# Optimization experiments

Hardware: AMD Instinct MI355X
Metric: run time of the kernel (lower is better)

The kernel has to match this reference:

```python
import jax, jax.numpy as jnp
import numpy as np

EPS = 1e-5
SLOPE = 0.01  # torch LeakyReLU default

def _conv(x, w, b, stride):
    # x: [B,C,L], w: [O,I,3]
    y = jax.lax.conv_general_dilated(x, w, (stride,), [(1, 1)],
                                     dimension_numbers=("NCH", "OIH", "NCH"))
    return y + b[None, :, None]

def _bn(x, g, b, m, v):
    # eval-mode BatchNorm1d with running stats
    inv = jax.lax.rsqrt(v + EPS)
    return (x - m[None, :, None]) * (g * inv)[None, :, None] + b[None, :, None]

def _lrelu(x):
    return jnp.where(x >= 0, x, SLOPE * x)

def setup_inputs() -> dict:
    key = jax.random.key(0)
    ks = jax.random.split(key, 32)
    B, C, L = 32, 256, 2048
    K, D = 4096, 128
    d = {}
    d["x"] = jax.random.normal(ks[0], (B, C, L), dtype=jnp.float32)
    # conv weights [O,I,3]
    d["w1"] = jax.random.normal(ks[1], (256, 256, 3), jnp.float32) * 0.03
    d["b1"] = jax.random.normal(ks[2], (256,), jnp.float32) * 0.01
    d["w2"] = jax.random.normal(ks[3], (512, 256, 3), jnp.float32) * 0.03
    d["b2"] = jax.random.normal(ks[4], (512,), jnp.float32) * 0.01
    d["w3"] = jax.random.normal(ks[5], (512, 512, 3), jnp.float32) * 0.02
    d["b3"] = jax.random.normal(ks[6], (512,), jnp.float32) * 0.01
    d["w4"] = jax.random.normal(ks[7], (D, 512, 3), jnp.float32) * 0.02
    d["b4"] = jax.random.normal(ks[8], (D,), jnp.float32) * 0.01
    for i, ch in enumerate([256, 512, 512, D]):
        d[f"g{i+1}"] = 1.0 + 0.1 * jax.random.normal(ks[9 + 4 * i], (ch,), jnp.float32)
        d[f"be{i+1}"] = 0.1 * jax.random.normal(ks[10 + 4 * i], (ch,), jnp.float32)
        d[f"m{i+1}"] = 0.1 * jax.random.normal(ks[11 + 4 * i], (ch,), jnp.float32)
        d[f"v{i+1}"] = 0.5 + jax.random.uniform(ks[12 + 4 * i], (ch,), jnp.float32)
    d["emb"] = jax.random.uniform(ks[30], (K, D), jnp.float32,
                                  minval=-1.0 / K, maxval=1.0 / K)
    return d

def reference(x, w1, b1, w2, b2, w3, b3, w4, b4,
              g1, be1, m1, v1, g2, be2, m2, v2,
              g3, be3, m3, v3, g4, be4, m4, v4, emb):
    h = _lrelu(_bn(_conv(x, w1, b1, 2), g1, be1, m1, v1))   # [B,256,L/2]
    h = _lrelu(_bn(_conv(h, w2, b2, 2), g2, be2, m2, v2))   # [B,512,L/4]
    h = _lrelu(_bn(_conv(h, w3, b3, 2), g3, be3, m3, v3))   # [B,512,L/8]
    h = _lrelu(_bn(_conv(h, w4, b4, 1), g4, be4, m4, v4))   # [B,D,L/8]
    flat = jnp.transpose(h, (0, 2, 1)).reshape(-1, h.shape[1])  # [N,D]
    # squared-distance expansion: ||f||^2 + ||e||^2 - 2 f.e
    dist = (jnp.sum(flat * flat, axis=1, keepdims=True)
            + jnp.sum(emb * emb, axis=1)
            - 2.0 * flat @ emb.T)                            # [N,K]
    codes = jnp.argmin(dist, axis=1)
    return codes, dist
```

## Files before the change

### kernel.cpp

```cpp
#include <hip/hip_runtime.h>
#include <cstdint>
#include <math.h>

#define EPS_BN 1e-5f
#define SLOPE 0.01f
#define C14 6.103515625e-5f
#define SC14 16384.0f
#define HMIN 6.103515625e-5f

typedef __attribute__((ext_vector_type(8))) _Float16 half8;
typedef __attribute__((ext_vector_type(8))) short short8;
typedef __attribute__((ext_vector_type(16))) float f32x16;
typedef __attribute__((ext_vector_type(4))) float f32x4;

__device__ __forceinline__ void split16(float v, unsigned short& uh,
                                        unsigned short& ul) {
    _Float16 h = (_Float16)v;
    if (fabsf(v) < HMIN) h = (_Float16)0.0f;
    float rem = v - (float)h;
    _Float16 l = (_Float16)(rem * SC14);
    uh = __builtin_bit_cast(unsigned short, h);
    ul = __builtin_bit_cast(unsigned short, l);
}

__global__ __launch_bounds__(256)
void wprep_all(const float* __restrict__ w1, short* __restrict__ o1,
               const float* __restrict__ w2, short* __restrict__ o2,
               const float* __restrict__ w3, short* __restrict__ o3,
               const float* __restrict__ w4, short* __restrict__ o4)
{
    const float* w; short* wbuf; int CIN, COUT;
    switch (blockIdx.y) {
        case 0: w = w1; wbuf = o1; CIN = 256; COUT = 256; break;
        case 1: w = w2; wbuf = o2; CIN = 256; COUT = 512; break;
        case 2: w = w3; wbuf = o3; CIN = 512; COUT = 512; break;
        default: w = w4; wbuf = o4; CIN = 512; COUT = 128; break;
    }
    int KST = CIN / 16, OB = COUT / 128;
    int total = KST * OB * 1536;
    for (int sid = blockIdx.x * 256 + threadIdx.x; sid < total;
         sid += gridDim.x * 256) {
        int slot = sid % 1536;
        int kb = sid / 1536;
        int ob = kb % OB, ks = kb / OB;
        int m = slot & 31, hi = (slot >> 5) & 1, mf = (slot >> 6) & 3;
        int ts = slot >> 8;
        int t = ts >> 1, s = ts & 1;
        int oc = ob * 128 + mf * 32 + m;
        int ib = ks * 16 + hi * 8;
        short8 r;
        #pragma unroll
        for (int j = 0; j < 8; ++j) {
            float v = w[((size_t)oc * CIN + ib + j) * 3 + t];
            unsigned short uh, ul;
            split16(v, uh, ul);
            r[j] = (short)(s == 0 ? uh : ul);
        }
        *(short8*)(wbuf + (size_t)sid * 8) = r;
    }
}

__global__ __launch_bounds__(256)
void bnprep_init(
    const float* __restrict__ g1, const float* __restrict__ be1,
    const float* __restrict__ m1, const float* __restrict__ v1,
    const float* __restrict__ b1, float* __restrict__ sc1, float* __restrict__ off1,
    const float* __restrict__ g2, const float* __restrict__ be2,
    const float* __restrict__ m2, const float* __restrict__ v2,
    const float* __restrict__ b2, float* __restrict__ sc2, float* __restrict__ off2,
    const float* __restrict__ g3, const float* __restrict__ be3,
    const float* __restrict__ m3, const float* __restrict__ v3,
    const float* __restrict__ b3, float* __restrict__ sc3, float* __restrict__ off3,
    const float* __restrict__ g4, const float* __restrict__ be4,
    const float* __restrict__ m4, const float* __restrict__ v4,
    const float* __restrict__ b4, float* __restrict__ sc4, float* __restrict__ off4,
    unsigned long long* __restrict__ mp, float* __restrict__ sf)
{
    int bid = blockIdx.x;
    if (bid >= 38) { sf[(bid - 38) * 256 + threadIdx.x] = 0.0f; return; }
    if (bid >= 6) { mp[(bid - 6) * 256 + threadIdx.x] = ~0ULL; return; }
    const float *g, *be, *m, *v, *bias;
    float *sc, *off;
    int c;
    if (bid == 0) {
        g = g1; be = be1; m = m1; v = v1; bias = b1; sc = sc1; off = off1;
        c = threadIdx.x;
    } else if (bid <= 2) {
        g = g2; be = be2; m = m2; v = v2; bias = b2; sc = sc2; off = off2;
        c = (bid - 1) * 256 + threadIdx.x;
    } else if (bid <= 4) {
        g = g3; be = be3; m = m3; v = v3; bias = b3; sc = sc3; off = off3;
        c = (bid - 3) * 256 + threadIdx.x;
    } else {
        g = g4; be = be4; m = m4; v = v4; bias = b4; sc = sc4; off = off4;
        c = threadIdx.x;
        if (c >= 128) return;
    }
    float s = g[c] / sqrtf(v[c] + EPS_BN);
    sc[c] = s;
    off[c] = (bias[c] - m[c]) * s + be[c];
}

template<int CIN, int COUT, int LIN, int TILE, int EPI, int SRC>
__global__ __launch_bounds__(512, 1)
void conv_pair(const short* __restrict__ wbuf, const short* __restrict__ xpl,
               const float* __restrict__ xraw,
               const float* __restrict__ scv, const float* __restrict__ offv,
               short* __restrict__ opl)
{
    constexpr int LOUT = LIN / 2;
    constexpr int KST = CIN / 16;
    constexpr int OBS = COUT / 128;
    constexpr int NG = CIN / 8;
    constexpr int SLOTS = LIN / 2 + 1;
    constexpr size_t PLIN = (size_t)32 * NG * 2 * SLOTS * 8;
    constexpr int NF = TILE / 64;
    constexpr int NGo = COUT / 8;
    constexpr int OSLOTS = (EPI == 0) ? (LOUT / 2 + 1) : (LOUT + 2);
    constexpr size_t PLOUT = (size_t)32 * NGo * ((EPI == 0) ? 2 : 1) * OSLOTS * 8;

    constexpr int XOFF = 49152;
    constexpr int BUF  = XOFF + 8 * 2112;
    constexpr int SCOFF = 2 * BUF;
    __shared__ __align__(16) char lds[2 * BUF + 2048];

    const int tid = threadIdx.x;
    const int lane = tid & 63;
    const int wv = tid >> 6;
    const int wo = wv >> 2;
    const int wm = (wv >> 1) & 1, wn = wv & 1;
    const int hi = lane >> 5, n32 = lane & 31;
    const int n0 = blockIdx.x * TILE;
    const int oby = blockIdx.y;
    const int o0 = oby * 256;
    const int b = blockIdx.z;

    if (tid < 256) ((float*)(lds + SCOFF))[tid] = scv[o0 + tid];
    else ((float*)(lds + SCOFF + 1024))[tid - 256] = offv[o0 + tid - 256];

    f32x16 acc0[2][2], acc1[2][2];
    #pragma unroll
    for (int i = 0; i < 2; ++i)
        #pragma unroll
        for (int j = 0; j < 2; ++j)
            #pragma unroll
            for (int e = 0; e < 16; ++e) { acc0[i][j][e] = 0.0f; acc1[i][j][e] = 0.0f; }

    short8 rw[6];
    short8 rxa, rxb, rxc;
    float rf[8], rf2[8];

    auto stage_load = [&](int ks) {
        const short* wsrc = wbuf + ((size_t)ks * OBS + (oby * 2 + wo)) * 1536 * 8;
        #pragma unroll
        for (int it = 0; it < 6; ++it)
            rw[it] = *(const short8*)(wsrc +
                      (size_t)(it * 256 + (wv & 3) * 64 + lane) * 8);
        if constexpr (SRC == 0) {
            int sg = wv >> 2, rhi = (wv >> 1) & 1, arr = wv & 1;
            int start = arr ? n0 : (n0 + 1);
            const short* src = xpl + (size_t)sg * PLIN
                + ((((size_t)b * NG + (ks * 2 + rhi)) * 2 + arr) * SLOTS + start) * 8;
            rxa = *(const short8*)(src + (size_t)lane * 8);
            if constexpr (TILE == 128) {
                rxb = *(const short8*)(src + (size_t)(64 + lane) * 8);
                if (arr && lane == 0)
                    rxc = *(const short8*)(src + (size_t)128 * 8);
            } else {
                if (arr && lane == 0)
                    rxb = *(const short8*)(src + (size_t)64 * 8);
            }
        } else {
            int run = wv & 3, rhi = run >> 1, arr = run & 1, hs = wv >> 2;
            int c = hs * 64 + lane;
            int l = arr ? (2 * (n0 + c) - 1) : (2 * (n0 + c));
            const float* xr = xraw + ((size_t)(b * 256 + ks * 16 + rhi * 8)) * 2048;
            #pragma unroll
            for (int j = 0; j < 8; ++j)
                rf[j] = (l >= 0) ? xr[(size_t)j * 2048 + l] : 0.0f;
            if (arr && hs == 1 && lane == 0) {
                int l2 = 2 * (n0 + 128) - 1;
                #pragma unroll
                for (int j = 0; j < 8; ++j)
                    rf2[j] = xr[(size_t)j * 2048 + l2];
            }
        }
    };

    auto stage_write = [&](char* base) {
        #pragma unroll
        for (int it = 0; it < 6; ++it)
            *(short8*)(base + wo * 24576 +
                       (it * 256 + (wv & 3) * 64 + lane) * 16) = rw[it];
        if constexpr (SRC == 0) {
            int sg = wv >> 2, rhi = (wv >> 1) & 1, arr = wv & 1;
            char* dst = base + XOFF + ((sg * 2 + rhi) * 2 + arr) * 2112;
            *(short8*)(dst + lane * 16) = rxa;
            if constexpr (TILE == 128) {
                *(short8*)(dst + (64 + lane) * 16) = rxb;
                if (arr && lane == 0) *(short8*)(dst + 128 * 16) = rxc;
            } else {
                if (arr && lane == 0) *(short8*)(dst + 64 * 16) = rxb;
            }
        } else {
            int run = wv & 3, rhi = run >> 1, arr = run & 1, hs = wv >> 2;
            int c = hs * 64 + lane;
            short8 rh, rl;
            #pragma unroll
            for (int j = 0; j < 8; ++j) {
                unsigned short uh, ul;
                split16(rf[j], uh, ul);
                rh[j] = (short)uh; rl[j] = (short)ul;
            }
            char* dst = base + XOFF + (rhi * 2 + arr) * 2112;
            *(short8*)(dst + c * 16) = rh;
            *(short8*)(dst + 8448 + c * 16) = rl;
            if (arr && hs == 1 && lane == 0) {
                short8 rh2, rl2;
                #pragma unroll
                for (int j = 0; j < 8; ++j) {
                    unsigned short uh, ul;
                    split16(rf2[j], uh, ul);
                    rh2[j] = (short)uh; rl2[j] = (short)ul;
                }
                *(short8*)(dst + 128 * 16) = rh2;
                *(short8*)(dst + 8448 + 128 * 16) = rl2;
            }
        }
    };

    stage_load(0);
    stage_write(lds);
    __syncthreads();

    #pragma unroll 1
    for (int ks = 0; ks < KST; ++ks) {
        const char* cbase = lds + (ks & 1) * BUF;
        bool more = (ks + 1 < KST);
        if (more) stage_load(ks + 1);
        __builtin_amdgcn_s_setprio(1);
        #pragma unroll
        for (int t = 0; t < 3; ++t) {
            half8 af[2][2], bx[2][2];
            #pragma unroll
            for (int s = 0; s < 2; ++s) {
                #pragma unroll
                for (int mf = 0; mf < 2; ++mf)
                    af[s][mf] = *(const half8*)(cbase + wo * 24576 +
                        (((t * 2 + s) * 4 + (wm * 2 + mf)) * 64 + lane) * 16);
                int arr = (t == 1) ? 0 : 1;
                int tof = (t == 2) ? 1 : 0;
                #pragma unroll
                for (int nf = 0; nf < NF; ++nf) {
                    int qb = wn * (TILE / 2) + nf * 32 + tof;
                    bx[s][nf] = *(const half8*)(cbase + XOFF + s * 8448
                                                + arr * 2112 + qb * 16
                                                + hi * 4224 + n32 * 16);
                }
            }
            #pragma unroll
            for (int mf = 0; mf < 2; ++mf)
                #pragma unroll
                for (int nf = 0; nf < NF; ++nf) {
                    acc0[mf][nf] = __builtin_amdgcn_mfma_f32_32x32x16_f16(
                        af[0][mf], bx[0][nf], acc0[mf][nf], 0, 0, 0);
                    acc1[mf][nf] = __builtin_amdgcn_mfma_f32_32x32x16_f16(
                        af[0][mf], bx[1][nf], acc1[mf][nf], 0, 0, 0);
                    acc1[mf][nf] = __builtin_amdgcn_mfma_f32_32x32x16_f16(
                        af[1][mf], bx[0][nf], acc1[mf][nf], 0, 0, 0);
                }
        }
        __builtin_amdgcn_s_setprio(0);
        if (more) stage_write(lds + ((ks + 1) & 1) * BUF);
        __syncthreads();
    }

    #pragma unroll
    for (int half = 0; half < NF; ++half) {
        __syncthreads();
        #pragma unroll
        for (int mf = 0; mf < 2; ++mf)
            #pragma unroll
            for (int r = 0; r < 16; ++r) {
                int ocl = mf * 32 + (r & 3) + 8 * (r >> 2) + 4 * hi;
                *(float*)(lds + wv * 8704 + n32 * 272 + ocl * 4) =
                    acc0[mf][half][r] + C14 * acc1[mf][half][r];
            }
        __syncthreads();
        #pragma unroll
        for (int it = 0; it < 4; ++it) {
            int sl = tid + it * 512;
            int w = sl >> 8, rem = sl & 255, p = rem >> 3, grp = rem & 7;
            int wo_ = w >> 2, wm_ = (w >> 1) & 1, wn_ = w & 1;
            f32x4 v0 = *(f32x4*)(lds + w * 8704 + p * 272 + grp * 32);
            f32x4 v1 = *(f32x4*)(lds + w * 8704 + p * 272 + grp * 32 + 16);
            int ocb = wo_ * 128 + wm_ * 64 + grp * 8;
            f32x4 s0 = *(f32x4*)(lds + SCOFF + ocb * 4);
            f32x4 s1 = *(f32x4*)(lds + SCOFF + ocb * 4 + 16);
            f32x4 q0 = *(f32x4*)(lds + SCOFF + 1024 + ocb * 4);
            f32x4 q1 = *(f32x4*)(lds + SCOFF + 1024 + ocb * 4 + 16);
            float y[8];
            #pragma unroll
            for (int j = 0; j < 4; ++j) {
                float a = v0[j] * s0[j] + q0[j];
                y[j] = a >= 0.0f ? a : SLOPE * a;
                float c = v1[j] * s1[j] + q1[j];
                y[4 + j] = c >= 0.0f ? c : SLOPE * c;
            }
            int pos_abs = n0 + wn_ * (TILE / 2) + half * 32 + p;
            int oc_abs = o0 + ocb;
            short8 rh, rl;
            #pragma unroll
            for (int j = 0; j < 8; ++j) {
                unsigned short uh, ul;
                split16(y[j], uh, ul);
                rh[j] = (short)uh; rl[j] = (short)ul;
            }
            int gq = oc_abs >> 3;
            size_t base;
            if (EPI == 0) {
                int arr = pos_abs & 1;
                int slot = arr ? (pos_abs + 1) / 2 : pos_abs / 2 + 1;
                base = ((((size_t)b * NGo + gq) * 2 + arr) * OSLOTS + slot) * 8;
            } else {
                base = (((size_t)b * NGo + gq) * OSLOTS + (pos_abs + 1)) * 8;
            }
            *(short8*)(opl + base) = rh;
            *(short8*)(opl + PLOUT + base) = rl;
        }
    }

    if (EPI == 0) {
        if (blockIdx.x == 0 && tid < 128) {
            int sg = tid >> 6, r2 = tid & 63, g16 = r2 >> 1, a2 = r2 & 1;
            int gq = oby * 32 + g16;
            short8 z;
            #pragma unroll
            for (int j = 0; j < 8; ++j) z[j] = 0;
            *(short8*)(opl + (size_t)sg * PLOUT +
                       ((((size_t)b * NGo + gq) * 2 + a2) * OSLOTS) * 8) = z;
        }
    } else {
        if (tid < 64 && (blockIdx.x == 0 || blockIdx.x == gridDim.x - 1)) {
            int sg = tid >> 5, g16 = tid & 31;
            int gq = oby * 32 + g16;
            int slot = (blockIdx.x == 0) ? 0 : (OSLOTS - 1);
            short8 z;
            #pragma unroll
            for (int j = 0; j < 8; ++j) z[j] = 0;
            *(short8*)(opl + (size_t)sg * PLOUT +
                       (((size_t)b * NGo + gq) * OSLOTS + slot) * 8) = z;
        }
    }
}

template<int CIN, int COUT, int LIN>
__global__ __launch_bounds__(256, 2)
void conv_s1(const short* __restrict__ wbuf, const short* __restrict__ xpl,
             const float* __restrict__ scv, const float* __restrict__ offv,
             short* __restrict__ fh, short* __restrict__ fl,
             float* __restrict__ sf)
{
    constexpr int KST = CIN / 16;
    constexpr int NG = CIN / 8;
    constexpr int SLOTS = LIN + 2;
    constexpr size_t PLIN = (size_t)32 * NG * SLOTS * 8;
    constexpr int TILE = 64;

    constexpr int XOFF = 24576;
    constexpr int BUF  = XOFF + 4 * 2112;
    constexpr int SCOFF = 2 * BUF;
    __shared__ __align__(16) char lds[2 * BUF + 1024];

    const int tid = threadIdx.x;
    const int lane = tid & 63;
    const int wv = tid >> 6;
    const int wm = wv >> 1, wn = wv & 1;
    const int hi = lane >> 5, n32 = lane & 31;
    const int n0 = blockIdx.x * TILE;
    const int b = blockIdx.z;

    if (tid < 128) {
        ((float*)(lds + SCOFF))[tid] = scv[tid];
        ((float*)(lds + SCOFF + 512))[tid] = offv[tid];
    }

    f32x16 acc0[2], acc1[2];
    #pragma unroll
    for (int i = 0; i < 2; ++i)
        #pragma unroll
        for (int e = 0; e < 16; ++e) { acc0[i][e] = 0.0f; acc1[i][e] = 0.0f; }

    short8 rw[6], rxa, rxb;

    auto stage_load = [&](int ks) {
        const short* wsrc = wbuf + (size_t)ks * 1536 * 8;
        #pragma unroll
        for (int it = 0; it < 6; ++it)
            rw[it] = *(const short8*)(wsrc +
                      (size_t)(it * 256 + wv * 64 + lane) * 8);
        int sg = wv >> 1, rhi = wv & 1;
        const short* src = xpl + (size_t)sg * PLIN
            + (((size_t)b * NG + (ks * 2 + rhi)) * SLOTS + n0) * 8;
        rxa = *(const short8*)(src + (size_t)lane * 8);
        if (lane < 2) rxb = *(const short8*)(src + (size_t)(64 + lane) * 8);
    };
    auto stage_write = [&](char* base) {
        #pragma unroll
        for (int it = 0; it < 6; ++it)
            *(short8*)(base + (it * 256 + wv * 64 + lane) * 16) = rw[it];
        int sg = wv >> 1, rhi = wv & 1;
        char* dst = base + XOFF + (sg * 2 + rhi) * 2112;
        *(short8*)(dst + lane * 16) = rxa;
        if (lane < 2) *(short8*)(dst + (64 + lane) * 16) = rxb;
    };

    stage_load(0);
    stage_write(lds);
    __syncthreads();

    #pragma unroll 1
    for (int ks = 0; ks < KST; ++ks) {
        const char* cbase = lds + (ks & 1) * BUF;
        bool more = (ks + 1 < KST);
        if (more) stage_load(ks + 1);
        __builtin_amdgcn_s_setprio(1);
        #pragma unroll
        for (int t = 0; t < 3; ++t) {
            half8 af[2][2], bx[2];
            #pragma unroll
            for (int s = 0; s < 2; ++s) {
                #pragma unroll
                for (int mf = 0; mf < 2; ++mf)
                    af[s][mf] = *(const half8*)(cbase +
                        (((t * 2 + s) * 4 + (wm * 2 + mf)) * 64 + lane) * 16);
                int qb = wn * 32 + t;
                bx[s] = *(const half8*)(cbase + XOFF + s * 4224
                                        + qb * 16 + hi * 2112 + n32 * 16);
            }
            #pragma unroll
            for (int mf = 0; mf < 2; ++mf) {
                acc0[mf] = __builtin_amdgcn_mfma_f32_32x32x16_f16(
                    af[0][mf], bx[0], acc0[mf], 0, 0, 0);
                acc1[mf] = __builtin_amdgcn_mfma_f32_32x32x16_f16(
                    af[0][mf], bx[1], acc1[mf], 0, 0, 0);
                acc1[mf] = __builtin_amdgcn_mfma_f32_32x32x16_f16(
                    af[1][mf], bx[0], acc1[mf], 0, 0, 0);
            }
        }
        __builtin_amdgcn_s_setprio(0);
        if (more) stage_write(lds + ((ks + 1) & 1) * BUF);
        __syncthreads();
    }

    __syncthreads();
    #pragma unroll
    for (int mf = 0; mf < 2; ++mf)
        #pragma unroll
        for (int r = 0; r < 16; ++r) {
            int ocl = mf * 32 + (r & 3) + 8 * (r >> 2) + 4 * hi;
            *(float*)(lds + wv * 8704 + n32 * 272 + ocl * 4) =
                acc0[mf][r] + C14 * acc1[mf][r];
        }
    __syncthreads();
    #pragma unroll
    for (int it = 0; it < 4; ++it) {
        int sl = tid + it * 256;
        int w = sl >> 8, rem = sl & 255, p = rem >> 3, grp = rem & 7;
        int wm_ = w >> 1, wn_ = w & 1;
        f32x4 v0 = *(f32x4*)(lds + w * 8704 + p * 272 + grp * 32);
        f32x4 v1 = *(f32x4*)(lds + w * 8704 + p * 272 + grp * 32 + 16);
        int oclb = wm_ * 64 + grp * 8;
        f32x4 s0 = *(f32x4*)(lds + SCOFF + oclb * 4);
        f32x4 s1 = *(f32x4*)(lds + SCOFF + oclb * 4 + 16);
        f32x4 q0 = *(f32x4*)(lds + SCOFF + 512 + oclb * 4);
        f32x4 q1 = *(f32x4*)(lds + SCOFF + 512 + oclb * 4 + 16);
        float y[8];
        #pragma unroll
        for (int j = 0; j < 4; ++j) {
            float a = v0[j] * s0[j] + q0[j];
            y[j] = a >= 0.0f ? a : SLOPE * a;
            float c = v1[j] * s1[j] + q1[j];
            y[4 + j] = c >= 0.0f ? c : SLOPE * c;
        }
        int pos_abs = n0 + wn_ * 32 + p;
        int n = b * 256 + pos_abs;
        short8 rh, rl;
        float partial = 0.0f;
        #pragma unroll
        for (int j = 0; j < 8; ++j) {
            partial = fmaf(y[j], y[j], partial);
            unsigned short uh, ul;
            split16(y[j], uh, ul);
            rh[j] = (short)uh; rl[j] = (short)ul;
        }
        int g = wm_ * 8 + grp;
        size_t slot = ((((size_t)(n >> 5) * 8 + (g >> 1)) * 2 + (g & 1)) * 32
                       + (n & 31)) * 8;
        *(short8*)(fh + slot) = rh;
        *(short8*)(fl + slot) = rl;
        atomicAdd(sf + n, partial);
    }
}

__global__ __launch_bounds__(256)
void split_kernel(const float* __restrict__ src, int nrows,
                  short* __restrict__ ph, short* __restrict__ pl,
                  float* __restrict__ sumv)
{
    int t = blockIdx.x * 256 + threadIdx.x;
    int n = t >> 4, g = t & 15;
    if (n >= nrows) return;
    const float* rowp = src + (size_t)n * 128 + g * 8;
    float4 v0 = *(const float4*)rowp;
    float4 v1 = *(const float4*)(rowp + 4);
    float vv[8] = {v0.x, v0.y, v0.z, v0.w, v1.x, v1.y, v1.z, v1.w};
    short8 rh, rl;
    float ss = 0.0f;
    #pragma unroll
    for (int j = 0; j < 8; ++j) {
        float v = vv[j];
        ss = fmaf(v, v, ss);
        unsigned short uh, ul;
        split16(v, uh, ul);
        rh[j] = (short)uh; rl[j] = (short)ul;
    }
    int nb = n >> 5, m = n & 31, ks = g >> 1, hi = g & 1;
    size_t slot = ((((size_t)nb * 8 + ks) * 2 + hi) * 32 + m) * 8;
    *(short8*)(ph + slot) = rh;
    *(short8*)(pl + slot) = rl;
    #pragma unroll
    for (int mk = 8; mk; mk >>= 1) ss += __shfl_xor(ss, mk);
    if (g == 0) sumv[n] = ss;
}

__global__ __launch_bounds__(256, 2)
void distmin_kernel(const short* __restrict__ fh, const short* __restrict__ fl,
                    const short* __restrict__ eh, const short* __restrict__ el,
                    const float* __restrict__ sf, const float* __restrict__ se,
                    float* __restrict__ dist, unsigned long long* __restrict__ mp)
{
    __shared__ unsigned long long cand[128 * 64];
    const int tid = threadIdx.x;
    const int lane = tid & 63;
    const int wv = tid >> 6;
    const int wm = wv >> 1, wn = wv & 1;
    const int hi = lane >> 5, n32 = lane & 31;
    const int kb = blockIdx.x;
    const int nb = blockIdx.y;

    f32x16 acc0[2][2], acc1[2][2];
    #pragma unroll
    for (int i = 0; i < 2; ++i)
        #pragma unroll
        for (int j = 0; j < 2; ++j)
            #pragma unroll
            for (int e = 0; e < 16; ++e) { acc0[i][j][e] = 0.0f; acc1[i][j][e] = 0.0f; }

    const short* fb[2][2];
    const short* eb[2][2];
    {
        const short* fpl[2] = {fh, fl};
        const short* epl[2] = {eh, el};
        #pragma unroll
        for (int s = 0; s < 2; ++s) {
            #pragma unroll
            for (int mf = 0; mf < 2; ++mf)
                fb[s][mf] = fpl[s] + (size_t)nb * 16384
                            + ((size_t)(wm * 2 + mf) * 8 * 64 + lane) * 8;
            #pragma unroll
            for (int nf = 0; nf < 2; ++nf)
                eb[s][nf] = epl[s]
                            + ((size_t)(kb * 4 + wn * 2 + nf) * 8 * 64 + lane) * 8;
        }
    }

    #pragma unroll
    for (int ks = 0; ks < 8; ++ks) {
        half8 af[2][2], bx[2][2];
        #pragma unroll
        for (int s = 0; s < 2; ++s) {
            #pragma unroll
            for (int mf = 0; mf < 2; ++mf)
                af[s][mf] = *(const half8*)(fb[s][mf] + ks * 512);
            #pragma unroll
            for (int nf = 0; nf < 2; ++nf)
                bx[s][nf] = *(const half8*)(eb[s][nf] + ks * 512);
        }
        #pragma unroll
        for (int mf = 0; mf < 2; ++mf)
            #pragma unroll
            for (int nf = 0; nf < 2; ++nf) {
                acc0[mf][nf] = __builtin_amdgcn_mfma_f32_32x32x16_f16(
                    af[0][mf], bx[0][nf], acc0[mf][nf], 0, 0, 0);
                acc1[mf][nf] = __builtin_amdgcn_mfma_f32_32x32x16_f16(
                    af[0][mf], bx[1][nf], acc1[mf][nf], 0, 0, 0);
                acc1[mf][nf] = __builtin_amdgcn_mfma_f32_32x32x16_f16(
                    af[1][mf], bx[0][nf], acc1[mf][nf], 0, 0, 0);
            }
    }

    const int n_blk = nb * 128;
    const int kc0 = kb * 128 + wn * 64 + n32;
    const float se0 = se[kc0];
    const float se1 = se[kc0 + 32];
    #pragma unroll
    for (int mf = 0; mf < 2; ++mf) {
        #pragma unroll
        for (int r = 0; r < 16; ++r) {
            int nloc = wm * 64 + mf * 32 + (r & 3) + 8 * (r >> 2) + 4 * hi;
            int n = n_blk + nloc;
            float sfn = sf[n];
            float d0 = acc0[mf][0][r] + C14 * acc1[mf][0][r];
            float d1 = acc0[mf][1][r] + C14 * acc1[mf][1][r];
            float v0 = (sfn + se0) - 2.0f * d0;
            float v1 = (sfn + se1) - 2.0f * d1;
            __builtin_nontemporal_store(v0, &dist[(size_t)n * 4096 + kc0]);
            __builtin_nontemporal_store(v1, &dist[(size_t)n * 4096 + kc0 + 32]);
            unsigned long long p0 =
                (((unsigned long long)__float_as_uint(v0)) << 32) | (unsigned)kc0;
            unsigned long long p1 =
                (((unsigned long long)__float_as_uint(v1)) << 32) | (unsigned)(kc0 + 32);
            unsigned long long p = p1 < p0 ? p1 : p0;
            cand[nloc * 64 + wn * 32 + n32] = p;
        }
    }
    __syncthreads();
    {
        int row = tid >> 1, h = tid & 1;
        unsigned long long best = ~0ULL;
        #pragma unroll
        for (int i = 0; i < 32; ++i) {
            int c = h * 32 + ((i + row) & 31);
            unsigned long long cv = cand[row * 64 + c];
            best = cv < best ? cv : best;
        }
        unsigned lo = (unsigned)best, hw = (unsigned)(best >> 32);
        unsigned lo2 = __shfl_xor(lo, 1), hw2 = __shfl_xor(hw, 1);
        unsigned long long ob = (((unsigned long long)hw2) << 32) | lo2;
        if (ob < best) best = ob;
        if (h == 0) atomicMin(mp + n_blk + row, best);
    }
}

__global__ __launch_bounds__(256)
void codes_kernel(const unsigned long long* __restrict__ mp,
                  float* __restrict__ codes)
{
    int n = blockIdx.x * 256 + threadIdx.x;
    if (n < 8192) codes[n] = (float)(unsigned)(mp[n] & 0xffffffffULL);
}

extern "C" void kernel_launch(void* const* d_in, const int* in_sizes, int n_in,
                              void* d_out, int out_size, void* d_ws, size_t ws_size,
                              hipStream_t stream)
{
    const float* x   = (const float*)d_in[0];
    const float* w1  = (const float*)d_in[1];
    const float* b1  = (const float*)d_in[2];
    const float* w2  = (const float*)d_in[3];
    const float* b2  = (const float*)d_in[4];
    const float* w3  = (const float*)d_in[5];
    const float* b3  = (const float*)d_in[6];
    const float* w4  = (const float*)d_in[7];
    const float* b4  = (const float*)d_in[8];
    const float* g1  = (const float*)d_in[9];
    const float* be1 = (const float*)d_in[10];
    const float* m1  = (const float*)d_in[11];
    const float* v1  = (const float*)d_in[12];
    const float* g2  = (const float*)d_in[13];
    const float* be2 = (const float*)d_in[14];
    const float* m2  = (const float*)d_in[15];
    const float* v2  = (const float*)d_in[16];
    const float* g3  = (const float*)d_in[17];
    const float* be3 = (const float*)d_in[18];
    const float* m3  = (const float*)d_in[19];
    const float* v3  = (const float*)d_in[20];
    const float* g4  = (const float*)d_in[21];
    const float* be4 = (const float*)d_in[22];
    const float* m4  = (const float*)d_in[23];
    const float* v4  = (const float*)d_in[24];
    const float* emb = (const float*)d_in[25];

    float* outf  = (float*)d_out;
    float* codes = outf;
    float* distm = outf + 8192;

    char* wsb = (char*)d_ws;
    short* wb1 = (short*)(wsb + 0);
    short* wb2 = (short*)(wsb + 786432);
    short* wb3 = (short*)(wsb + 2359296);
    short* wb4 = (short*)(wsb + 5505024);
    float* sc1 = (float*)(wsb + 6291456); float* off1 = sc1 + 256;
    float* sc2 = (float*)(wsb + 6293504); float* off2 = sc2 + 512;
    float* sc3 = (float*)(wsb + 6297600); float* off3 = sc3 + 512;
    float* sc4 = (float*)(wsb + 6301696); float* off4 = sc4 + 128;
    short* h1p = (short*)(wsb + 6302720);
    short* fh  = (short*)(wsb + 39922688);
    short* fl  = (short*)(wsb + 42019840);
    short* eh  = (short*)(wsb + 44116992);
    short* el  = (short*)(wsb + 45165568);
    float* sf  = (float*)(wsb + 46214144);
    float* se  = (float*)(wsb + 46246912);
    unsigned long long* mp = (unsigned long long*)(wsb + 46263296);

    char* db = (char*)distm;
    short* h2p = (short*)db;
    short* h3p = (short*)(db + 33685504);

    wprep_all<<<dim3(192, 4), 256, 0, stream>>>(w1, wb1, w2, wb2, w3, wb3, w4, wb4);
    bnprep_init<<<70, 256, 0, stream>>>(
        g1, be1, m1, v1, b1, sc1, off1,
        g2, be2, m2, v2, b2, sc2, off2,
        g3, be3, m3, v3, b3, sc3, off3,
        g4, be4, m4, v4, b4, sc4, off4, mp, sf);
    split_kernel<<<256, 256, 0, stream>>>(emb, 4096, eh, el, se);

    conv_pair<256, 256, 2048, 128, 0, 1>
        <<<dim3(8, 1, 32), 512, 0, stream>>>(wb1, nullptr, x, sc1, off1, h1p);
    conv_pair<256, 512, 1024, 128, 0, 0>
        <<<dim3(4, 2, 32), 512, 0, stream>>>(wb2, h1p, nullptr, sc2, off2, h2p);
    conv_pair<512, 512, 512, 64, 1, 0>
        <<<dim3(4, 2, 32), 512, 0, stream>>>(wb3, h2p, nullptr, sc3, off3, h3p);
    conv_s1<512, 128, 256>
        <<<dim3(4, 1, 32), 256, 0, stream>>>(wb4, h3p, sc4, off4, fh, fl, sf);

    distmin_kernel<<<dim3(32, 64), 256, 0, stream>>>(fh, fl, eh, el,
                                                     sf, se, distm, mp);
    codes_kernel<<<32, 256, 0, stream>>>(mp, codes);
}
```

Baseline: 235.1 us.

## Replace LDS-staged conv kernels with a direct-global-load generalized conv kernel

Generalizes the stride-1 conv kernel into conv_ng, which handles stride-2 and stride-1 layers with configurable tile and epilogue, and uses it for conv layers 2-4 in place of conv_pair and conv_s1. The main loop no longer double-buffers weights and activations through shared memory; each wave loads its MFMA fragments straight from global memory, relying on cache, and unrolls by two. Output channels are split across blockIdx.y in 128-wide blocks, with 256-thread blocks instead of 512. This removes LDS staging and barriers from the K loop, at the cost of redundant global or L2 traffic and more exposed load latency.

Result: slower. 306.8 us (+30.5%).

```diff
diff --git a/kernel.cpp b/kernel.cpp
--- a/kernel.cpp
+++ b/kernel.cpp
@@ -354,23 +354,28 @@
     }
 }
 
-template<int CIN, int COUT, int LIN>
-__global__ __launch_bounds__(256, 2)
-void conv_s1(const short* __restrict__ wbuf, const short* __restrict__ xpl,
+template<int CIN, int COUT, int LIN, int STRIDE, int TILE, int EPI>
+__global__ __launch_bounds__(256)
+void conv_ng(const short* __restrict__ wbuf, const short* __restrict__ xpl,
              const float* __restrict__ scv, const float* __restrict__ offv,
-             short* __restrict__ fh, short* __restrict__ fl,
-             float* __restrict__ sf)
+             short* __restrict__ opl, short* __restrict__ fh,
+             short* __restrict__ fl, float* __restrict__ sf)
 {
+    constexpr int LOUT = LIN / STRIDE;
     constexpr int KST = CIN / 16;
+    constexpr int OBS = COUT / 128;
     constexpr int NG = CIN / 8;
-    constexpr int SLOTS = LIN + 2;
-    constexpr size_t PLIN = (size_t)32 * NG * SLOTS * 8;
-    constexpr int TILE = 64;
-
-    constexpr int XOFF = 24576;
-    constexpr int BUF  = XOFF + 4 * 2112;
-    constexpr int SCOFF = 2 * BUF;
-    __shared__ __align__(16) char lds[2 * BUF + 1024];
+    constexpr int NARR = (STRIDE == 2) ? 2 : 1;
+    constexpr int SLOTS = (STRIDE == 2) ? (LIN / 2 + 1) : (LIN + 2);
+    constexpr size_t PLIN = (size_t)32 * NG * NARR * SLOTS * 8;
+    constexpr int PW = TILE / 2;
+    constexpr int NF = PW / 32;
+    constexpr int NGo = COUT / 8;
+    constexpr int OSLOTS = (EPI == 0) ? (LOUT / 2 + 1) : (LOUT + 2);
+    constexpr size_t PLOUT = (size_t)32 * NGo * ((EPI == 0) ? 2 : 1) * OSLOTS * 8;
+
+    constexpr int SCOFF = 4 * 8704;
+    __shared__ __align__(16) char lds[SCOFF + 1024];
 
     const int tid = threadIdx.x;
     const int lane = tid & 63;
@@ -378,128 +383,158 @@
     const int wm = wv >> 1, wn = wv & 1;
     const int hi = lane >> 5, n32 = lane & 31;
     const int n0 = blockIdx.x * TILE;
+    const int ob = blockIdx.y;
+    const int o0 = ob * 128;
     const int b = blockIdx.z;
 
     if (tid < 128) {
-        ((float*)(lds + SCOFF))[tid] = scv[tid];
-        ((float*)(lds + SCOFF + 512))[tid] = offv[tid];
-    }
-
-    f32x16 acc0[2], acc1[2];
+        ((float*)(lds + SCOFF))[tid] = scv[o0 + tid];
+        ((float*)(lds + SCOFF + 512))[tid] = offv[o0 + tid];
+    }
+
+    f32x16 acc0[2][NF], acc1[2][NF];
     #pragma unroll
     for (int i = 0; i < 2; ++i)
         #pragma unroll
-        for (int e = 0; e < 16; ++e) { acc0[i][e] = 0.0f; acc1[i][e] = 0.0f; }
-
-    short8 rw[6], rxa, rxb;
-
-    auto stage_load = [&](int ks) {
-        const short* wsrc = wbuf + (size_t)ks * 1536 * 8;
-        #pragma unroll
-        for (int it = 0; it < 6; ++it)
-            rw[it] = *(const short8*)(wsrc +
-                      (size_t)(it * 256 + wv * 64 + lane) * 8);
-        int sg = wv >> 1, rhi = wv & 1;
-        const short* src = xpl + (size_t)sg * PLIN
-            + (((size_t)b * NG + (ks * 2 + rhi)) * SLOTS + n0) * 8;
-        rxa = *(const short8*)(src + (size_t)lane * 8);
-        if (lane < 2) rxb = *(const short8*)(src + (size_t)(64 + lane) * 8);
-    };
-    auto stage_write = [&](char* base) {
-        #pragma unroll
-        for (int it = 0; it < 6; ++it)
-            *(short8*)(base + (it * 256 + wv * 64 + lane) * 16) = rw[it];
-        int sg = wv >> 1, rhi = wv & 1;
-        char* dst = base + XOFF + (sg * 2 + rhi) * 2112;
-        *(short8*)(dst + lane * 16) = rxa;
-        if (lane < 2) *(short8*)(dst + (64 + lane) * 16) = rxb;
-    };
-
-    stage_load(0);
-    stage_write(lds);
-    __syncthreads();
-
-    #pragma unroll 1
+        for (int j = 0; j < NF; ++j)
+            #pragma unroll
+            for (int e = 0; e < 16; ++e) { acc0[i][j][e] = 0.0f; acc1[i][j][e] = 0.0f; }
+
+    const short* wb = wbuf + ((size_t)ob * 1536 + wm * 128 + lane) * 8;
+    constexpr size_t WKS = (size_t)OBS * 1536 * 8;
+
+    size_t xslot0;
+    if constexpr (STRIDE == 2)
+        xslot0 = ((size_t)(b * NG + hi) * 2) * SLOTS + n0 + wn * PW + n32;
+    else
+        xslot0 = ((size_t)(b * NG + hi)) * SLOTS + n0 + wn * PW + n32;
+    const short* xb = xpl + xslot0 * 8;
+    constexpr size_t XKS = (size_t)((STRIDE == 2) ? 4 : 2) * SLOTS * 8;
+
+    #pragma unroll 2
     for (int ks = 0; ks < KST; ++ks) {
-        const char* cbase = lds + (ks & 1) * BUF;
-        bool more = (ks + 1 < KST);
-        if (more) stage_load(ks + 1);
-        __builtin_amdgcn_s_setprio(1);
+        const short* wk = wb + (size_t)ks * WKS;
+        const short* xk = xb + (size_t)ks * XKS;
+        half8 af[3][2][2], bx[3][2][NF];
         #pragma unroll
         for (int t = 0; t < 3; ++t) {
-            half8 af[2][2], bx[2];
+            constexpr int XT2[3] = {SLOTS, 1, SLOTS + 1};
+            int xt = (STRIDE == 2) ? XT2[t] : t;
             #pragma unroll
             for (int s = 0; s < 2; ++s) {
                 #pragma unroll
                 for (int mf = 0; mf < 2; ++mf)
-                    af[s][mf] = *(const half8*)(cbase +
-                        (((t * 2 + s) * 4 + (wm * 2 + mf)) * 64 + lane) * 16);
-                int qb = wn * 32 + t;
-                bx[s] = *(const half8*)(cbase + XOFF + s * 4224
-                                        + qb * 16 + hi * 2112 + n32 * 16);
-            }
-            #pragma unroll
-            for (int mf = 0; mf < 2; ++mf) {
-                acc0[mf] = __builtin_amdgcn_mfma_f32_32x32x16_f16(
-                    af[0][mf], bx[0], acc0[mf], 0, 0, 0);
-                acc1[mf] = __builtin_amdgcn_mfma_f32_32x32x16_f16(
-                    af[0][mf], bx[1], acc1[mf], 0, 0, 0);
-                acc1[mf] = __builtin_amdgcn_mfma_f32_32x32x16_f16(
-                    af[1][mf], bx[0], acc1[mf], 0, 0, 0);
-            }
-        }
-        __builtin_amdgcn_s_setprio(0);
-        if (more) stage_write(lds + ((ks + 1) & 1) * BUF);
+                    af[t][s][mf] = *(const half8*)(wk +
+                        ((size_t)((t * 2 + s) * 256 + mf * 64)) * 8);
+                #pragma unroll
+                for (int nf = 0; nf < NF; ++nf)
+                    bx[t][s][nf] = *(const half8*)(xk + (size_t)s * PLIN
+                                                   + (size_t)(xt + nf * 32) * 8);
+            }
+        }
+        #pragma unroll
+        for (int t = 0; t < 3; ++t)
+            #pragma unroll
+            for (int mf = 0; mf < 2; ++mf)
+                #pragma unroll
+                for (int nf = 0; nf < NF; ++nf) {
+                    acc0[mf][nf] = __builtin_amdgcn_mfma_f32_32x32x16_f16(
+                        af[t][0][mf], bx[t][0][nf], acc0[mf][nf], 0, 0, 0);
+                    acc1[mf][nf] = __builtin_amdgcn_mfma_f32_32x32x16_f16(
+                        af[t][0][mf], bx[t][1][nf], acc1[mf][nf], 0, 0, 0);
+                    acc1[mf][nf] = __builtin_amdgcn_mfma_f32_32x32x16_f16(
+                        af[t][1][mf], bx[t][0][nf], acc1[mf][nf], 0, 0, 0);
+                }
+    }
+
+    #pragma unroll
+    for (int half = 0; half < NF; ++half) {
         __syncthreads();
-    }
-
-    __syncthreads();
-    #pragma unroll
-    for (int mf = 0; mf < 2; ++mf)
-        #pragma unroll
-        for (int r = 0; r < 16; ++r) {
-            int ocl = mf * 32 + (r & 3) + 8 * (r >> 2) + 4 * hi;
-            *(float*)(lds + wv * 8704 + n32 * 272 + ocl * 4) =
-                acc0[mf][r] + C14 * acc1[mf][r];
-        }
-    __syncthreads();
-    #pragma unroll
-    for (int it = 0; it < 4; ++it) {
-        int sl = tid + it * 256;
-        int w = sl >> 8, rem = sl & 255, p = rem >> 3, grp = rem & 7;
-        int wm_ = w >> 1, wn_ = w & 1;
-        f32x4 v0 = *(f32x4*)(lds + w * 8704 + p * 272 + grp * 32);
-        f32x4 v1 = *(f32x4*)(lds + w * 8704 + p * 272 + grp * 32 + 16);
-        int oclb = wm_ * 64 + grp * 8;
-        f32x4 s0 = *(f32x4*)(lds + SCOFF + oclb * 4);
-        f32x4 s1 = *(f32x4*)(lds + SCOFF + oclb * 4 + 16);
-        f32x4 q0 = *(f32x4*)(lds + SCOFF + 512 + oclb * 4);
-        f32x4 q1 = *(f32x4*)(lds + SCOFF + 512 + oclb * 4 + 16);
-        float y[8];
-        #pragma unroll
-        for (int j = 0; j < 4; ++j) {
-            float a = v0[j] * s0[j] + q0[j];
-            y[j] = a >= 0.0f ? a : SLOPE * a;
-            float c = v1[j] * s1[j] + q1[j];
-            y[4 + j] = c >= 0.0f ? c : SLOPE * c;
-        }
-        int pos_abs = n0 + wn_ * 32 + p;
-        int n = b * 256 + pos_abs;
-        short8 rh, rl;
-        float partial = 0.0f;
-        #pragma unroll
-        for (int j = 0; j < 8; ++j) {
-            partial = fmaf(y[j], y[j], partial);
-            unsigned short uh, ul;
-            split16(y[j], uh, ul);
-            rh[j] = (short)uh; rl[j] = (short)ul;
-        }
-        int g = wm_ * 8 + grp;
-        size_t slot = ((((size_t)(n >> 5) * 8 + (g >> 1)) * 2 + (g & 1)) * 32
-                       + (n & 31)) * 8;
-        *(short8*)(fh + slot) = rh;
-        *(short8*)(fl + slot) = rl;
-        atomicAdd(sf + n, partial);
+        #pragma unroll
+        for (int mf = 0; mf < 2; ++mf)
+            #pragma unroll
+            for (int r = 0; r < 16; ++r) {
+                int ocl = mf * 32 + (r & 3) + 8 * (r >> 2) + 4 * hi;
+                *(float*)(lds + wv * 8704 + n32 * 272 + ocl * 4) =
+                    acc0[mf][half][r] + C14 * acc1[mf][half][r];
+            }
+        __syncthreads();
+        #pragma unroll
+        for (int it = 0; it < 4; ++it) {
+            int sl = tid + it * 256;
+            int w = sl >> 8, rem = sl & 255, p = rem >> 3, grp = rem & 7;
+            int wm_ = w >> 1, wn_ = w & 1;
+            f32x4 v0 = *(f32x4*)(lds + w * 8704 + p * 272 + grp * 32);
+            f32x4 v1 = *(f32x4*)(lds + w * 8704 + p * 272 + grp * 32 + 16);
+            int ocb = wm_ * 64 + grp * 8;
+            f32x4 s0 = *(f32x4*)(lds + SCOFF + ocb * 4);
+            f32x4 s1 = *(f32x4*)(lds + SCOFF + ocb * 4 + 16);
+            f32x4 q0 = *(f32x4*)(lds + SCOFF + 512 + ocb * 4);
+            f32x4 q1 = *(f32x4*)(lds + SCOFF + 512 + ocb * 4 + 16);
+            float y[8];
+            #pragma unroll
+            for (int j = 0; j < 4; ++j) {
+                float a = v0[j] * s0[j] + q0[j];
+                y[j] = a >= 0.0f ? a : SLOPE * a;
+                float c = v1[j] * s1[j] + q1[j];
+                y[4 + j] = c >= 0.0f ? c : SLOPE * c;
+            }
+            int pos_abs = n0 + wn_ * PW + half * 32 + p;
+            int oc_abs = o0 + ocb;
+            short8 rh, rl;
+            float partial = 0.0f;
+            #pragma unroll
+            for (int j = 0; j < 8; ++j) {
+                if (EPI == 2) partial = fmaf(y[j], y[j], partial);
+                unsigned short uh, ul;
+                split16(y[j], uh, ul);
+                rh[j] = (short)uh; rl[j] = (short)ul;
+            }
+            if constexpr (EPI == 2) {
+                int n = b * 256 + pos_abs;
+                int g = oc_abs >> 3;
+                size_t slot = ((((size_t)(n >> 5) * 8 + (g >> 1)) * 2 + (g & 1)) * 32
+                               + (n & 31)) * 8;
+                *(short8*)(fh + slot) = rh;
+                *(short8*)(fl + slot) = rl;
+                atomicAdd(sf + n, partial);
+            } else {
+                int gq = oc_abs >> 3;
+                size_t base;
+                if (EPI == 0) {
+                    int arr = pos_abs & 1;
+                    int slot = arr ? (pos_abs + 1) / 2 : pos_abs / 2 + 1;
+                    base = ((((size_t)b * NGo + gq) * 2 + arr) * OSLOTS + slot) * 8;
+                } else {
+                    base = (((size_t)b * NGo + gq) * OSLOTS + (pos_abs + 1)) * 8;
+                }
+                *(short8*)(opl + base) = rh;
+                *(short8*)(opl + PLOUT + base) = rl;
+            }
+        }
+    }
+
+    if constexpr (EPI == 0) {
+        if (blockIdx.x == 0 && tid < 64) {
+            int sg = tid >> 5, r2 = tid & 31, g16 = r2 >> 1, a2 = r2 & 1;
+            int gq = ob * 16 + g16;
+            short8 z;
+            #pragma unroll
+            for (int j = 0; j < 8; ++j) z[j] = 0;
+            *(short8*)(opl + (size_t)sg * PLOUT +
+                       ((((size_t)b * NGo + gq) * 2 + a2) * OSLOTS) * 8) = z;
+        }
+    } else if constexpr (EPI == 1) {
+        if (tid < 32 && (blockIdx.x == 0 || blockIdx.x == gridDim.x - 1)) {
+            int sg = tid >> 4, g16 = tid & 15;
+            int gq = ob * 16 + g16;
+            int slot = (blockIdx.x == 0) ? 0 : (OSLOTS - 1);
+            short8 z;
+            #pragma unroll
+            for (int j = 0; j < 8; ++j) z[j] = 0;
+            *(short8*)(opl + (size_t)sg * PLOUT +
+                       (((size_t)b * NGo + gq) * OSLOTS + slot) * 8) = z;
+        }
     }
 }
 
@@ -718,12 +753,15 @@
 
     conv_pair<256, 256, 2048, 128, 0, 1>
         <<<dim3(8, 1, 32), 512, 0, stream>>>(wb1, nullptr, x, sc1, off1, h1p);
-    conv_pair<256, 512, 1024, 128, 0, 0>
-        <<<dim3(4, 2, 32), 512, 0, stream>>>(wb2, h1p, nullptr, sc2, off2, h2p);
-    conv_pair<512, 512, 512, 64, 1, 0>
-        <<<dim3(4, 2, 32), 512, 0, stream>>>(wb3, h2p, nullptr, sc3, off3, h3p);
-    conv_s1<512, 128, 256>
-        <<<dim3(4, 1, 32), 256, 0, stream>>>(wb4, h3p, sc4, off4, fh, fl, sf);
+    conv_ng<256, 512, 1024, 2, 128, 0>
+        <<<dim3(4, 4, 32), 256, 0, stream>>>(wb2, h1p, sc2, off2, h2p,
+                                             nullptr, nullptr, nullptr);
+    conv_ng<512, 512, 512, 2, 128, 1>
+        <<<dim3(2, 4, 32), 256, 0, stream>>>(wb3, h2p, sc3, off3, h3p,
+                                             nullptr, nullptr, nullptr);
+    conv_ng<512, 128, 256, 1, 64, 2>
+        <<<dim3(4, 1, 32), 256, 0, stream>>>(wb4, h3p, sc4, off4, nullptr,
+                                             fh, fl, sf);
 
     distmin_kernel<<<dim3(32, 64), 256, 0, stream>>>(fh, fl, eh, el,
                                                      sf, se, distm, mp);
```

## Load conv weight fragments directly from global memory instead of staging through LDS

Applied to the files above, without the earlier changes.

Both conv kernels stop staging the weight tile through registers into double-buffered shared memory. Each wave now reads its MFMA A-fragments straight from global memory inside the inner loop, and only the activation tile stays in LDS. This removes the weight LDS writes and reads and shrinks the shared-memory footprint. In exchange, weight loads are no longer prefetched one stage ahead, so global or L2 latency lands directly in the MFMA loop, and waves sharing weights issue redundant global reads.

Result: slower. 313.1 us (+33.2%).

```diff
diff --git a/kernel.cpp b/kernel.cpp
--- a/kernel.cpp
+++ b/kernel.cpp
@@ -119,10 +119,9 @@
     constexpr int OSLOTS = (EPI == 0) ? (LOUT / 2 + 1) : (LOUT + 2);
     constexpr size_t PLOUT = (size_t)32 * NGo * ((EPI == 0) ? 2 : 1) * OSLOTS * 8;
 
-    constexpr int XOFF = 49152;
-    constexpr int BUF  = XOFF + 8 * 2112;
-    constexpr int SCOFF = 2 * BUF;
-    __shared__ __align__(16) char lds[2 * BUF + 2048];
+    constexpr int BUF  = 8 * 2112;
+    constexpr int SCOFF = 8 * 8704;
+    __shared__ __align__(16) char lds[SCOFF + 2048];
 
     const int tid = threadIdx.x;
     const int lane = tid & 63;
@@ -146,16 +145,13 @@
             #pragma unroll
             for (int e = 0; e < 16; ++e) { acc0[i][j][e] = 0.0f; acc1[i][j][e] = 0.0f; }
 
-    short8 rw[6];
+    const short* wkb = wbuf + ((size_t)(oby * 2 + wo) * 1536 + lane) * 8;
+    constexpr size_t WKS = (size_t)OBS * 1536 * 8;
+
     short8 rxa, rxb, rxc;
     float rf[8], rf2[8];
 
     auto stage_load = [&](int ks) {
-        const short* wsrc = wbuf + ((size_t)ks * OBS + (oby * 2 + wo)) * 1536 * 8;
-        #pragma unroll
-        for (int it = 0; it < 6; ++it)
-            rw[it] = *(const short8*)(wsrc +
-                      (size_t)(it * 256 + (wv & 3) * 64 + lane) * 8);
         if constexpr (SRC == 0) {
             int sg = wv >> 2, rhi = (wv >> 1) & 1, arr = wv & 1;
             int start = arr ? n0 : (n0 + 1);
@@ -188,13 +184,9 @@
     };
 
     auto stage_write = [&](char* base) {
-        #pragma unroll
-        for (int it = 0; it < 6; ++it)
-            *(short8*)(base + wo * 24576 +
-                       (it * 256 + (wv & 3) * 64 + lane) * 16) = rw[it];
         if constexpr (SRC == 0) {
             int sg = wv >> 2, rhi = (wv >> 1) & 1, arr = wv & 1;
-            char* dst = base + XOFF + ((sg * 2 + rhi) * 2 + arr) * 2112;
+            char* dst = base + ((sg * 2 + rhi) * 2 + arr) * 2112;
             *(short8*)(dst + lane * 16) = rxa;
             if constexpr (TILE == 128) {
                 *(short8*)(dst + (64 + lane) * 16) = rxb;
@@ -212,7 +204,7 @@
                 split16(rf[j], uh, ul);
                 rh[j] = (short)uh; rl[j] = (short)ul;
             }
-            char* dst = base + XOFF + (rhi * 2 + arr) * 2112;
+            char* dst = base + (rhi * 2 + arr) * 2112;
             *(short8*)(dst + c * 16) = rh;
             *(short8*)(dst + 8448 + c * 16) = rl;
             if (arr && hs == 1 && lane == 0) {
@@ -236,6 +228,7 @@
     #pragma unroll 1
     for (int ks = 0; ks < KST; ++ks) {
         const char* cbase = lds + (ks & 1) * BUF;
+        const short* wk = wkb + (size_t)ks * WKS;
         bool more = (ks + 1 < KST);
         if (more) stage_load(ks + 1);
         __builtin_amdgcn_s_setprio(1);
@@ -246,14 +239,14 @@
             for (int s = 0; s < 2; ++s) {
                 #pragma unroll
                 for (int mf = 0; mf < 2; ++mf)
-                    af[s][mf] = *(const half8*)(cbase + wo * 24576 +
-                        (((t * 2 + s) * 4 + (wm * 2 + mf)) * 64 + lane) * 16);
+                    af[s][mf] = *(const half8*)(wk +
+                        (size_t)(((t * 2 + s) * 4 + (wm * 2 + mf)) * 64) * 8);
                 int arr = (t == 1) ? 0 : 1;
                 int tof = (t == 2) ? 1 : 0;
                 #pragma unroll
                 for (int nf = 0; nf < NF; ++nf) {
                     int qb = wn * (TILE / 2) + nf * 32 + tof;
-                    bx[s][nf] = *(const half8*)(cbase + XOFF + s * 8448
+                    bx[s][nf] = *(const half8*)(cbase + s * 8448
                                                 + arr * 2112 + qb * 16
                                                 + hi * 4224 + n32 * 16);
                 }
@@ -367,10 +360,9 @@
     constexpr size_t PLIN = (size_t)32 * NG * SLOTS * 8;
     constexpr int TILE = 64;
 
-    constexpr int XOFF = 24576;
-    constexpr int BUF  = XOFF + 4 * 2112;
-    constexpr int SCOFF = 2 * BUF;
-    __shared__ __align__(16) char lds[2 * BUF + 1024];
+    constexpr int BUF  = 4 * 2112;
+    constexpr int SCOFF = 4 * 8704;
+    __shared__ __align__(16) char lds[SCOFF + 1024];
 
     const int tid = threadIdx.x;
     const int lane = tid & 63;
@@ -391,14 +383,10 @@
         #pragma unroll
         for (int e = 0; e < 16; ++e) { acc0[i][e] = 0.0f; acc1[i][e] = 0.0f; }
 
-    short8 rw[6], rxa, rxb;
+    const short* wkb = wbuf + (size_t)lane * 8;
+    short8 rxa, rxb;
 
     auto stage_load = [&](int ks) {
-        const short* wsrc = wbuf + (size_t)ks * 1536 * 8;
-        #pragma unroll
-        for (int it = 0; it < 6; ++it)
-            rw[it] = *(const short8*)(wsrc +
-                      (size_t)(it * 256 + wv * 64 + lane) * 8);
         int sg = wv >> 1, rhi = wv & 1;
         const short* src = xpl + (size_t)sg * PLIN
             + (((size_t)b * NG + (ks * 2 + rhi)) * SLOTS + n0) * 8;
@@ -406,11 +394,8 @@
         if (lane < 2) rxb = *(const short8*)(src + (size_t)(64 + lane) * 8);
     };
     auto stage_write = [&](char* base) {
-        #pragma unroll
-        for (int it = 0; it < 6; ++it)
-            *(short8*)(base + (it * 256 + wv * 64 + lane) * 16) = rw[it];
         int sg = wv >> 1, rhi = wv & 1;
-        char* dst = base + XOFF + (sg * 2 + rhi) * 2112;
+        char* dst = base + (sg * 2 + rhi) * 2112;
         *(short8*)(dst + lane * 16) = rxa;
         if (lane < 2) *(short8*)(dst + (64 + lane) * 16) = rxb;
     };
@@ -422,6 +407,7 @@
     #pragma unroll 1
     for (int ks = 0; ks < KST; ++ks) {
         const char* cbase = lds + (ks & 1) * BUF;
+        const short* wk = wkb + (size_t)ks * 1536 * 8;
         bool more = (ks + 1 < KST);
         if (more) stage_load(ks + 1);
         __builtin_amdgcn_s_setprio(1);
@@ -432,10 +418,10 @@
             for (int s = 0; s < 2; ++s) {
                 #pragma unroll
                 for (int mf = 0; mf < 2; ++mf)
-                    af[s][mf] = *(const half8*)(cbase +
-                        (((t * 2 + s) * 4 + (wm * 2 + mf)) * 64 + lane) * 16);
+                    af[s][mf] = *(const half8*)(wk +
+                        (size_t)(((t * 2 + s) * 4 + (wm * 2 + mf)) * 64) * 8);
                 int qb = wn * 32 + t;
-                bx[s] = *(const half8*)(cbase + XOFF + s * 4224
+                bx[s] = *(const half8*)(cbase + s * 4224
                                         + qb * 16 + hi * 2112 + n32 * 16);
             }
             #pragma unroll
```
